# Performance work log

Measured on AMD Instinct MI355X. Metric: run time of the kernel, lower is better.

The kernel has to match this reference:

```python
import jax, jax.numpy as jnp
import numpy as np

# Reconstructed laminar V1-V2 dynamics (submodule sources were not provided;
# dynamics follow the documented dependency order L4 -> PV -> V2 -> template -> SOM -> L2/3).
N = 36            # n_orientations
H = 128           # v2_hidden_dim
DT_TAU = 0.1      # dt/tau for rate units
DT_TAU_A = 0.02   # dt/tau for adaptation
BETA_A = 0.5      # adaptation strength
W_PV = 1.0        # PV (divisive-ish subtractive) inhibition weight
W_SOM = 0.8       # SOM inhibition weight
FB_GAIN = 0.5     # feedback center-excitation gain
ALPHA = 1.0       # error-signal template subtraction
FB_SCALE = 1.0    # feedback_scale buffer


def _ring_kernel(key, n, scale):
    return scale * jax.random.normal(key, (n, n), dtype=jnp.float32)


def setup_inputs() -> dict:
    key = jax.random.key(0)
    ks = jax.random.split(key, 16)
    B, T = 1024, 512
    D_in = 2 * N + 2  # 74 packed width
    s = 1.0 / np.sqrt(N)
    sh = 1.0 / np.sqrt(D_in + H)
    return {
        "packed_input": jax.random.normal(ks[0], (B, T, D_in), dtype=jnp.float32),
        "W_l4": _ring_kernel(ks[1], N, s),
        "W_l23": _ring_kernel(ks[2], N, s),
        "W_som": _ring_kernel(ks[3], N, s),
        "Wz": sh * jax.random.normal(ks[4], (D_in + H, H), dtype=jnp.float32),
        "Wr": sh * jax.random.normal(ks[5], (D_in + H, H), dtype=jnp.float32),
        "Wh": sh * jax.random.normal(ks[6], (D_in + H, H), dtype=jnp.float32),
        "bz": jnp.zeros((H,), jnp.float32),
        "br": jnp.zeros((H,), jnp.float32),
        "bh": jnp.zeros((H,), jnp.float32),
        "Wq": (1.0 / np.sqrt(H)) * jax.random.normal(ks[7], (H, N), dtype=jnp.float32),
        "bq": jnp.zeros((N,), jnp.float32),
        "Wp": (1.0 / np.sqrt(H)) * jax.random.normal(ks[8], (H, 1), dtype=jnp.float32),
        "bp": jnp.zeros((1,), jnp.float32),
        "Ws": (1.0 / np.sqrt(H)) * jax.random.normal(ks[9], (H, 3), dtype=jnp.float32),
        "bs": jnp.zeros((3,), jnp.float32),
    }


def _forward(packed_input, W_l4, W_l23, W_som, Wz, Wr, Wh, bz, br, bh,
             Wq, bq, Wp, bp, Ws, bs):
    B, T, _ = packed_input.shape
    stim_seq = packed_input[..., :N]          # [B,T,N]
    cue_seq = packed_input[..., N:2 * N]      # [B,T,N]
    task_seq = packed_input[..., 2 * N:]      # [B,T,2]

    def gru(x, h):
        xh = jnp.concatenate([x, h], axis=-1)
        z = jax.nn.sigmoid(xh @ Wz + bz)
        r = jax.nn.sigmoid(xh @ Wr + br)
        xrh = jnp.concatenate([x, r * h], axis=-1)
        hh = jnp.tanh(xrh @ Wh + bh)
        return (1.0 - z) * h + z * hh

    def step(state, inp):
        r_l4, r_l23, r_pv, r_som, adapt, h_v2 = state
        stimulus, cue, task_state = inp
        # --- V1 L4 ring (with adaptation, PV inhibition) ---
        drive_l4 = stimulus + r_l4 @ W_l4.T - W_PV * r_pv - adapt
        r_l4_n = r_l4 + DT_TAU * (-r_l4 + jax.nn.relu(drive_l4))
        adapt_n = adapt + DT_TAU_A * (-adapt + BETA_A * r_l4_n)
        # --- PV pool (single unit per batch) ---
        pv_in = jnp.mean(r_l4_n, axis=-1, keepdims=True) + jnp.mean(r_l23, axis=-1, keepdims=True)
        r_pv_n = r_pv + DT_TAU * (-r_pv + jax.nn.relu(pv_in))
        # --- V2 context module (uses r_l23 at t-1) ---
        v2_in = jnp.concatenate([r_l23, cue, task_state], axis=-1)  # [B,74]
        h_v2_n = gru(v2_in, h_v2)
        q_pred = jax.nn.softmax(h_v2_n @ Wq + bq, axis=-1)          # [B,N]
        pi_raw = jax.nn.sigmoid(h_v2_n @ Wp + bp)                   # [B,1]
        state_logits = h_v2_n @ Ws + bs                              # [B,3]
        pi_eff = pi_raw * FB_SCALE
        # --- deep template + feedback signals ---
        deep_tmpl = q_pred * pi_eff
        som_drive = q_pred * pi_eff
        r_som_n = r_som + DT_TAU * (-r_som + jax.nn.relu(som_drive + r_som @ W_som.T))
        tmpl_mod = 1.0 + FB_GAIN * q_pred * pi_eff
        l4_to_l23 = r_l4_n - ALPHA * deep_tmpl
        # --- V1 L2/3 ring ---
        drive_l23 = l4_to_l23 * tmpl_mod + r_l23 @ W_l23.T - W_SOM * r_som_n - W_PV * r_pv_n
        r_l23_n = r_l23 + DT_TAU * (-r_l23 + jax.nn.relu(drive_l23))
        new_state = (r_l4_n, r_l23_n, r_pv_n, r_som_n, adapt_n, h_v2_n)
        return new_state, r_l23_n

    z = jnp.zeros((B, N), jnp.float32)
    init = (z, z, jnp.zeros((B, 1), jnp.float32), z, z, jnp.zeros((B, H), jnp.float32))
    inputs = (jnp.swapaxes(stim_seq, 0, 1), jnp.swapaxes(cue_seq, 0, 1), jnp.swapaxes(task_seq, 0, 1))
    _, r_l23_all = jax.lax.scan(step, init, inputs)  # [T,B,N]
    return jnp.swapaxes(r_l23_all, 0, 1)             # [B,T,N]


def reference(packed_input, W_l4, W_l23, W_som, Wz, Wr, Wh, bz, br, bh,
              Wq, bq, Wp, bp, Ws, bs):
    return _forward(packed_input, W_l4, W_l23, W_som, Wz, Wr, Wh, bz, br, bh,
                    Wq, bq, Wp, bp, Ws, bs)
```

## Files before the change

### kernel.cpp

```cpp
#include <hip/hip_runtime.h>
#include <cstdint>
#include <cstddef>


#define NN   36
#define HH   128
#define DIN  74
#define KT   202
#define KP   232
#define TT   512
#define RPB  4
#define NPAD 40
#define WSTR 44
#define HSTR 136
#define S2   6

typedef short bf16x8 __attribute__((ext_vector_type(8)));
typedef float f32x4  __attribute__((ext_vector_type(4)));

#define MFMA(a,b,c) __builtin_amdgcn_mfma_f32_16x16x32_bf16((a),(b),(c),0,0,0)
#define BAR() asm volatile("s_waitcnt lgkmcnt(0)\n\ts_barrier" ::: "memory")

__device__ __forceinline__ float fastrcp(float x) { return __builtin_amdgcn_rcpf(x); }
__device__ __forceinline__ float sigmf(float x) { return fastrcp(1.0f + __expf(-x)); }
__device__ __forceinline__ float tanhf_fast(float x) {
    return 1.0f - 2.0f * fastrcp(1.0f + __expf(2.0f * x));
}

__device__ __forceinline__ short f2bf(float v) {
    union { float f; unsigned u; } x; x.f = v;
    unsigned r = (x.u + 0x7fffu + ((x.u >> 16) & 1u)) >> 16;
    return (short)r;
}
__device__ __forceinline__ float bf2f(short s) {
    union { unsigned u; float f; } y; y.u = ((unsigned)(unsigned short)s) << 16;
    return y.f;
}

__device__ __forceinline__ unsigned cvtpk(float a, float b) {
    unsigned r;
    asm("v_cvt_pk_bf16_f32 %0, %1, %2" : "=v"(r) : "v"(a), "v"(b));
    return r;
}
__device__ __forceinline__ float lo16f(unsigned p) { return __uint_as_float(p << 16); }
__device__ __forceinline__ float hi16f(unsigned p) { return __uint_as_float(p & 0xffff0000u); }

#define DPP_STEP_MAX(x, ctrl) \
    x = fmaxf(x, __int_as_float(__builtin_amdgcn_update_dpp(0, __float_as_int(x), (ctrl), 0xF, 0xF, true)))
#define DPP_STEP_SUM(x, ctrl) \
    x = x + __int_as_float(__builtin_amdgcn_update_dpp(0, __float_as_int(x), (ctrl), 0xF, 0xF, true))

__device__ __forceinline__ float red16_max(float x) {
    DPP_STEP_MAX(x, 0xB1);
    DPP_STEP_MAX(x, 0x4E);
    DPP_STEP_MAX(x, 0x141);
    DPP_STEP_MAX(x, 0x140);
    return x;
}
__device__ __forceinline__ float red16_sum(float x) {
    DPP_STEP_SUM(x, 0xB1);
    DPP_STEP_SUM(x, 0x4E);
    DPP_STEP_SUM(x, 0x141);
    DPP_STEP_SUM(x, 0x140);
    return x;
}

#define HEADBASE 86016
#define FRAG_TOTAL 92160

extern "C" __global__ void __launch_bounds__(256)
init_frags(const float* __restrict__ Wz, const float* __restrict__ Wr,
           const float* __restrict__ Wh, const float* __restrict__ Wq,
           const float* __restrict__ Wp, short* __restrict__ frag)
{
    int idx = blockIdx.x * 256 + threadIdx.x;
    if (idx >= FRAG_TOTAL) return;
    float v;
    if (idx < HEADBASE) {
        int T = idx / 3584; int rem = idx - T * 3584;
        int s = rem >> 9;   int e = rem & 511;
        int l = e >> 3, j = e & 7;
        int k = s * 32 + ((l >> 4) << 3) + j;
        int n = ((T & 7) << 4) + (l & 15);
        const float* W = (T < 8) ? Wz : (T < 16) ? Wr : Wh;
        v = (k < KT) ? W[k * HH + n] : 0.f;
    } else {
        int r2 = idx - HEADBASE;
        int ts = r2 >> 9; int e = r2 & 511;
        int t = ts >> 2, s = ts & 3;
        int l = e >> 3, j = e & 7;
        int k = s * 32 + ((l >> 4) << 3) + j;
        int c = (t << 4) + (l & 15);
        v = (c < NN) ? Wq[k * NN + c] : (c == NN ? Wp[k] : 0.f);
    }
    frag[idx] = f2bf(v);
}

extern "C" __global__ void __launch_bounds__(1024, 4)
laminar_kernel(const float* __restrict__ packed,
               const float* __restrict__ Wl4,
               const float* __restrict__ Wl23,
               const float* __restrict__ Wsom,
               const float* __restrict__ bz,
               const float* __restrict__ br,
               const float* __restrict__ bh,
               const float* __restrict__ bq,
               const float* __restrict__ bp,
               const short* __restrict__ frag,
               float* __restrict__ out)
{
    const int tid  = threadIdx.x;
    const int r0   = blockIdx.x * RPB;
    const int lane = tid & 63;
    const int w    = tid >> 6;
    const int m    = lane & 15;
    const int q    = lane >> 4;
    const int arow = m & 7;
    const int ab   = arow >> 1;
    const int ap   = arow & 1;
    const int b0i  = (q & 1) << 1;
    const int b1i  = b0i + 1;

    __shared__ __align__(16) short xa[2][RPB][KP];
    __shared__ __align__(16) short xb[2][RPB][KP];
    __shared__ __align__(16) short hb[2][RPB][HSTR];
    __shared__ float hS[HH][S2];
    __shared__ float zgS[HH][S2];
    __shared__ float preq[48][S2];
    __shared__ __align__(16) float Wl4S[NN * WSTR], Wl23S[NN * WSTR], WsomS[NN * WSTR];
    __shared__ __align__(16) float l4s[RPB][NPAD], l23s[RPB][NPAD];
    __shared__ __align__(16) float soms[RPB][NPAD], adL[RPB][NPAD];
    __shared__ __align__(16) float l4part[RPB][NPAD];
    __shared__ __align__(16) float l23dotS[RPB][NPAD];
    __shared__ __align__(16) float somdotS[RPB][NPAD];
    __shared__ float bzL[HH], brL[HH], bhL[HH], bqL[48];
    __shared__ float pvL[RPB];
    __shared__ float bpS;

    for (int i = tid; i < HH; i += 1024) { bzL[i] = bz[i]; brL[i] = br[i]; bhL[i] = bh[i]; }
    for (int i = tid; i < 48; i += 1024) bqL[i] = (i < NN) ? bq[i] : 0.f;
    if (tid == 0) bpS = bp[0];
    for (int idx = tid; idx < NN * NN; idx += 1024) {
        const int i = idx / NN, j = idx - i * NN;
        Wl4S[i * WSTR + j]  = Wl4[idx];
        Wl23S[i * WSTR + j] = Wl23[idx];
        WsomS[i * WSTR + j] = Wsom[idx];
    }
    { short* p = (short*)xa; for (int i = tid; i < 2*RPB*KP; i += 1024) p[i] = 0; }
    { short* p = (short*)xb; for (int i = tid; i < 2*RPB*KP; i += 1024) p[i] = 0; }
    { short* p = (short*)hb; for (int i = tid; i < 2*RPB*HSTR; i += 1024) p[i] = 0; }
    { float* p = (float*)hS; for (int i = tid; i < HH*S2; i += 1024) p[i] = 0.f; }
    { float* p = (float*)l4s; for (int i = tid; i < RPB*NPAD; i += 1024) {
        p[i] = 0.f; ((float*)l23s)[i] = 0.f; ((float*)soms)[i] = 0.f;
        ((float*)adL)[i] = 0.f; ((float*)l23dotS)[i] = 0.f; ((float*)somdotS)[i] = 0.f; } }
    if (tid < RPB) pvL[tid] = 0.f;
    if (tid < RPB * NN) {
        const int r = tid / NN, i = tid - (tid / NN) * NN;
        l4part[r][i] = packed[((size_t)(r0 + r) * TT + 0) * DIN + i];
    }

    bf16x8 FA[7], FB[7];
    if (w < 8) {
        const short* a0 = frag + (w * 7) * 512 + lane * 8;
        const short* b0 = frag + ((8 + w) * 7) * 512 + lane * 8;
        #pragma unroll
        for (int s = 0; s < 7; ++s) {
            FA[s] = *(const bf16x8*)(a0 + s * 512);
            FB[s] = *(const bf16x8*)(b0 + s * 512);
        }
    } else {
        const int hw8 = w - 8;
        const short* a0 = frag + ((16 + hw8) * 7) * 512 + lane * 8;
        #pragma unroll
        for (int s = 0; s < 7; ++s) FA[s] = *(const bf16x8*)(a0 + s * 512);
        const int hw = (hw8 < 3) ? hw8 : 0;
        const short* b0 = frag + HEADBASE + (hw * 4) * 512 + lane * 8;
        #pragma unroll
        for (int s = 0; s < 4; ++s) FB[s] = *(const bf16x8*)(b0 + s * 512);
        FB[4] = FA[4]; FB[5] = FA[5]; FB[6] = FA[6];
    }

    const int  idA   = (w - 8) * 64 + lane;
    const bool isDotA = (w >= 8 && w < 11) && (idA < 144);
    const int  dvA = isDotA ? idA : 0;
    const int  drA = dvA / 36, diA = dvA - drA * 36;
    const float* dAW = Wl23S + diA * WSTR;
    const float* dAS = &l23s[drA][0];
    float*       dAD = &l23dotS[drA][diA];
    const int  idB   = (w - 13) * 64 + lane;
    const bool isL4f = (w >= 13) && (idB < 144);
    const int  lvB = isL4f ? idB : 0;
    const int  lr = lvB / 36, li = lvB - (lvB / 36) * 36;
    const int  idC   = w * 64 + lane;
    const bool isDotC = (w < 3) && (idC < 144);
    const int  cvC = isDotC ? idC : 0;
    const int  crC = cvC / 36, ciC = cvC - crC * 36;
    const float* dCW = WsomS + ciC * WSTR;
    const float* dCS = &soms[crC][0];
    float*       dCD = &somdotS[crC][ciC];
    const int  idD   = (w - 3) * 64 + lane;
    const bool isL4p = (w >= 3 && w < 6) && (idD < 144);
    const int  pvD = isL4p ? idD : 0;
    const int  prD = pvD / 36, piD = pvD - prD * 36;
    const float* pW = Wl4S + piD * WSTR;
    const float* pS = &l4s[prD][0];
    float*       pD = &l4part[prD][piD];
    const int  idE   = (w - 6) * 64 + lane;
    const bool isCue = (w >= 6 && w < 8) && (idE < 76);
    const int  evE = isCue ? idE : 0;
    const int  ctr = evE / 19;
    const int  ctc = 36 + 2 * (evE - ctr * 19);

    float ctv0 = 0.f, ctv1 = 0.f, stimreg = 0.f;
    if (isCue) {
        const size_t base0 = ((size_t)(r0 + ctr) * TT + 0) * DIN;
        #pragma unroll
        for (int d = 0; d < 2; ++d) {
            const float v = packed[base0 + ctc + d];
            const short hi = f2bf(v), lo = f2bf(v - bf2f(hi));
            xa[0][ctr][ctc + d] = hi; xa[1][ctr][ctc + d] = lo;
            if (ctc + d >= 64) { xb[0][ctr][ctc + d] = hi; xb[1][ctr][ctc + d] = lo; }
        }
        const size_t base1 = ((size_t)(r0 + ctr) * TT + 1) * DIN;
        ctv0 = packed[base1 + ctc]; ctv1 = packed[base1 + ctc + 1];
    }
    if (isL4f) stimreg = packed[((size_t)(r0 + lr) * TT + 1) * DIN + li];
    __syncthreads();

    for (int t = 0; t < TT; ++t) {
        if (w < 8) {
            const short* xaRow = &xa[ap][ab][0];
            bf16x8 Ax[7];
            #pragma unroll
            for (int s = 0; s < 7; ++s)
                Ax[s] = *(const bf16x8*)&xaRow[s * 32 + q * 8];
            f32x4 az = {0.f,0.f,0.f,0.f}, ar = {0.f,0.f,0.f,0.f};
            #pragma unroll
            for (int s = 0; s < 7; ++s) {
                az = MFMA(Ax[s], FA[s], az);
                ar = MFMA(Ax[s], FB[s], ar);
            }
            if (lane < 32) {
                const int f = w * 16 + m;
                const float z0 = az[0] + az[1], z1 = az[2] + az[3];
                const float r0v = ar[0] + ar[1], r1v = ar[2] + ar[3];
                zgS[f][b0i] = sigmf(z0 + bzL[f]);
                zgS[f][b1i] = sigmf(z1 + bzL[f]);
                const float ra = sigmf(r0v + brL[f]) * hS[f][b0i];
                const float rb = sigmf(r1v + brL[f]) * hS[f][b1i];
                const unsigned ph = cvtpk(ra, rb);
                const unsigned pl = cvtpk(ra - lo16f(ph), rb - hi16f(ph));
                xb[0][b0i][DIN + f] = (short)ph;         xb[1][b0i][DIN + f] = (short)pl;
                xb[0][b1i][DIN + f] = (short)(ph >> 16); xb[1][b1i][DIN + f] = (short)(pl >> 16);
            }
        } else if (isDotA) {
            float acc = 0.f;
            #pragma unroll
            for (int j = 0; j < NN; j += 4) {
                const float4 sv = *(const float4*)&dAS[j];
                const float4 wv = *(const float4*)&dAW[j];
                acc += sv.x*wv.x + sv.y*wv.y + sv.z*wv.z + sv.w*wv.w;
            }
            *dAD = acc;
        } else if (isL4f) {
            const float nl4 = 0.9f * l4s[lr][li]
                            + 0.1f * fmaxf(l4part[lr][li] - pvL[lr], 0.f);
            l4s[lr][li] = nl4;
            const float ad = 0.98f * adL[lr][li] + 0.01f * nl4;
            adL[lr][li] = ad;
            l4part[lr][li] = stimreg - ad;
            const int tn = (t + 2 < TT) ? t + 2 : TT - 1;
            stimreg = packed[((size_t)(r0 + lr) * TT + tn) * DIN + li];
        }
        BAR();

        if (w >= 8) {
            const short* xaRow = &xa[ap][ab][0];
            const short* xbRow = &xb[ap][ab][0];
            bf16x8 Op[7];
            Op[0] = *(const bf16x8*)&xaRow[q * 8];
            Op[1] = *(const bf16x8*)&xaRow[32 + q * 8];
            #pragma unroll
            for (int s = 2; s < 7; ++s)
                Op[s] = *(const bf16x8*)&xbRow[s * 32 + q * 8];
            f32x4 a = {0.f,0.f,0.f,0.f}, b = {0.f,0.f,0.f,0.f};
            a = MFMA(Op[0], FA[0], a);
            b = MFMA(Op[1], FA[1], b);
            a = MFMA(Op[2], FA[2], a);
            b = MFMA(Op[3], FA[3], b);
            a = MFMA(Op[4], FA[4], a);
            b = MFMA(Op[5], FA[5], b);
            a = MFMA(Op[6], FA[6], a);
            a = a + b;
            if (lane < 32) {
                const int f = (w - 8) * 16 + m;
                const float s0 = a[0] + a[1], s1 = a[2] + a[3];
                const float hh0 = tanhf_fast(s0 + bhL[f]);
                const float hh1 = tanhf_fast(s1 + bhL[f]);
                const float zg0 = zgS[f][b0i], zg1 = zgS[f][b1i];
                const float hn0 = (1.0f - zg0) * hS[f][b0i] + zg0 * hh0;
                const float hn1 = (1.0f - zg1) * hS[f][b1i] + zg1 * hh1;
                hS[f][b0i] = hn0; hS[f][b1i] = hn1;
                const unsigned ph = cvtpk(hn0, hn1);
                const unsigned pl = cvtpk(hn0 - lo16f(ph), hn1 - hi16f(ph));
                hb[0][b0i][f] = (short)ph;         hb[1][b0i][f] = (short)pl;
                hb[0][b1i][f] = (short)(ph >> 16); hb[1][b1i][f] = (short)(pl >> 16);
                xa[0][b0i][DIN + f] = (short)ph;         xa[1][b0i][DIN + f] = (short)pl;
                xa[0][b1i][DIN + f] = (short)(ph >> 16); xa[1][b1i][DIN + f] = (short)(pl >> 16);
            }
        } else if (isDotC) {
            float acc = 0.f;
            #pragma unroll
            for (int j = 0; j < NN; j += 4) {
                const float4 sv = *(const float4*)&dCS[j];
                const float4 wv = *(const float4*)&dCW[j];
                acc += sv.x*wv.x + sv.y*wv.y + sv.z*wv.z + sv.w*wv.w;
            }
            *dCD = acc;
        } else if (w == 6) {
            const int row = q;
            float s = l4s[row][m] + l23s[row][m] + l4s[row][m + 16] + l23s[row][m + 16];
            if (m < 4) s += l4s[row][m + 32] + l23s[row][m + 32];
            s = red16_sum(s);
            if (m == 0) pvL[row] = 0.9f * pvL[row] + 0.1f * fmaxf(s * (1.0f / 36.0f), 0.f);
        }
        BAR();

        if (w >= 8 && w < 11) {
            const short* hbRow = &hb[ap][ab][0];
            bf16x8 Hk[4];
            #pragma unroll
            for (int s = 0; s < 4; ++s)
                Hk[s] = *(const bf16x8*)&hbRow[s * 32 + q * 8];
            f32x4 a = {0.f,0.f,0.f,0.f};
            #pragma unroll
            for (int s = 0; s < 4; ++s) a = MFMA(Hk[s], FB[s], a);
            if (lane < 32) {
                const int c = (w - 8) * 16 + m;
                preq[c][b0i] = a[0] + a[1];
                preq[c][b1i] = a[2] + a[3];
            }
        } else if (isL4p) {
            float acc = *pD;
            #pragma unroll
            for (int j = 0; j < NN; j += 4) {
                const float4 sv = *(const float4*)&pS[j];
                const float4 wv = *(const float4*)&pW[j];
                acc += sv.x*wv.x + sv.y*wv.y + sv.z*wv.z + sv.w*wv.w;
            }
            *pD = acc;
        } else if (isCue) {
            const unsigned ph = cvtpk(ctv0, ctv1);
            const unsigned pl = cvtpk(ctv0 - lo16f(ph), ctv1 - hi16f(ph));
            xa[0][ctr][ctc]     = (short)ph;         xa[1][ctr][ctc]     = (short)pl;
            xa[0][ctr][ctc + 1] = (short)(ph >> 16); xa[1][ctr][ctc + 1] = (short)(pl >> 16);
            if (ctc >= 64) {
                xb[0][ctr][ctc]     = (short)ph;         xb[1][ctr][ctc]     = (short)pl;
                xb[0][ctr][ctc + 1] = (short)(ph >> 16); xb[1][ctr][ctc + 1] = (short)(pl >> 16);
            }
            const int tn = (t + 2 < TT) ? t + 2 : TT - 1;
            const size_t base = ((size_t)(r0 + ctr) * TT + tn) * DIN;
            ctv0 = packed[base + ctc]; ctv1 = packed[base + ctc + 1];
        }
        BAR();

        if (w < 4) {
            const int rr = w;
            const float v0 = preq[m][rr] + bqL[m];
            const float v1 = preq[m + 16][rr] + bqL[m + 16];
            const float v2 = (m < 4) ? (preq[m + 32][rr] + bqL[m + 32]) : -1e30f;
            const float pi = sigmf(preq[36][rr] + bpS);
            const float mx = red16_max(fmaxf(fmaxf(v0, v1), v2));
            const float e0 = __expf(v0 - mx);
            const float e1 = __expf(v1 - mx);
            const float e2 = (m < 4) ? __expf(v2 - mx) : 0.f;
            const float ss = red16_sum(e0 + e1 + e2);
            const float sc = fastrcp(ss) * pi;
            if (lane < 16) {
                const float pv = pvL[rr];
                const size_t outb = ((size_t)(r0 + rr) * TT + t) * NN;
                float ln01[2];
                #pragma unroll
                for (int t2 = 0; t2 < 2; ++t2) {
                    const int i = m + 16 * t2;
                    const float dt = (t2 ? e1 : e0) * sc;
                    const float sn = 0.9f * soms[rr][i]
                                   + 0.1f * fmaxf(dt + somdotS[rr][i], 0.f);
                    soms[rr][i] = sn;
                    const float acc2 = (l4s[rr][i] - dt) * (1.0f + 0.5f * dt)
                                     + l23dotS[rr][i] - 0.8f * sn - pv;
                    const float ln = 0.9f * l23s[rr][i] + 0.1f * fmaxf(acc2, 0.f);
                    l23s[rr][i] = ln;
                    out[outb + i] = ln;
                    ln01[t2] = ln;
                }
                const unsigned ph = cvtpk(ln01[0], ln01[1]);
                const unsigned pl = cvtpk(ln01[0] - lo16f(ph), ln01[1] - hi16f(ph));
                xa[0][rr][m]      = (short)ph;         xa[1][rr][m]      = (short)pl;
                xa[0][rr][m + 16] = (short)(ph >> 16); xa[1][rr][m + 16] = (short)(pl >> 16);
                if (m < 4) {
                    const int i = m + 32;
                    const float dt = e2 * sc;
                    const float sn = 0.9f * soms[rr][i]
                                   + 0.1f * fmaxf(dt + somdotS[rr][i], 0.f);
                    soms[rr][i] = sn;
                    const float acc2 = (l4s[rr][i] - dt) * (1.0f + 0.5f * dt)
                                     + l23dotS[rr][i] - 0.8f * sn - pv;
                    const float ln = 0.9f * l23s[rr][i] + 0.1f * fmaxf(acc2, 0.f);
                    l23s[rr][i] = ln;
                    out[outb + i] = ln;
                    const short hi2 = f2bf(ln);
                    xa[0][rr][i] = hi2; xa[1][rr][i] = f2bf(ln - bf2f(hi2));
                }
            }
        }
        BAR();
    }
}

extern "C" void kernel_launch(void* const* d_in, const int* in_sizes, int n_in,
                              void* d_out, int out_size, void* d_ws, size_t ws_size,
                              hipStream_t stream) {
    (void)in_sizes; (void)n_in; (void)out_size; (void)ws_size;
    const float* packed = (const float*)d_in[0];
    const float* Wl4    = (const float*)d_in[1];
    const float* Wl23   = (const float*)d_in[2];
    const float* Wsom   = (const float*)d_in[3];
    const float* Wz     = (const float*)d_in[4];
    const float* Wr     = (const float*)d_in[5];
    const float* Wh     = (const float*)d_in[6];
    const float* bz     = (const float*)d_in[7];
    const float* br     = (const float*)d_in[8];
    const float* bh     = (const float*)d_in[9];
    const float* Wq     = (const float*)d_in[10];
    const float* bq     = (const float*)d_in[11];
    const float* Wp     = (const float*)d_in[12];
    const float* bp     = (const float*)d_in[13];
    float* out  = (float*)d_out;
    short* frag = (short*)d_ws;

    init_frags<<<(FRAG_TOTAL + 255) / 256, 256, 0, stream>>>(Wz, Wr, Wh, Wq, Wp, frag);
    laminar_kernel<<<256, 1024, 0, stream>>>(packed, Wl4, Wl23, Wsom,
                                             bz, br, bh, bq, bp, frag, out);
}
```

Baseline: 1.520 ms.

## Precompute non-recurrent GRU gate partials ahead of the step and rebalance wave roles

The z/r and candidate gate GEMMs are split so the K-chunks that do not depend on the hidden state from this step (cue/task and previous h) are accumulated in the previous phase. Only the two stimulus chunks are multiplied on the critical path. The ring matrices are stored in a 4-wide transposed layout for float4 dot products. Dot-product, L4 and cue-packing duties are reassigned across waves to balance the phases. This shortens the serial chain per timestep, at the cost of more complex role bookkeeping and some redundant MFMAs on the upper waves.

```diff
diff --git a/kernel.cpp b/kernel.cpp
--- a/kernel.cpp
+++ b/kernel.cpp
@@ -11,8 +11,7 @@
 #define TT   512
 #define RPB  4
 #define NPAD 40
-#define WSTR 44
-#define HSTR 136
+#define HSTR 144
 #define S2   6
 
 typedef short bf16x8 __attribute__((ext_vector_type(8)));
@@ -123,11 +122,11 @@
 
     __shared__ __align__(16) short xa[2][RPB][KP];
     __shared__ __align__(16) short xb[2][RPB][KP];
-    __shared__ __align__(16) short hb[2][RPB][HSTR];
+    __shared__ __align__(16) short hbS[2][RPB][HSTR];
     __shared__ float hS[HH][S2];
     __shared__ float zgS[HH][S2];
     __shared__ float preq[48][S2];
-    __shared__ __align__(16) float Wl4S[NN * WSTR], Wl23S[NN * WSTR], WsomS[NN * WSTR];
+    __shared__ __align__(16) float W4l4[1296], W4l23[1296], W4som[1296];
     __shared__ __align__(16) float l4s[RPB][NPAD], l23s[RPB][NPAD];
     __shared__ __align__(16) float soms[RPB][NPAD], adL[RPB][NPAD];
     __shared__ __align__(16) float l4part[RPB][NPAD];
@@ -140,24 +139,24 @@
     for (int i = tid; i < HH; i += 1024) { bzL[i] = bz[i]; brL[i] = br[i]; bhL[i] = bh[i]; }
     for (int i = tid; i < 48; i += 1024) bqL[i] = (i < NN) ? bq[i] : 0.f;
     if (tid == 0) bpS = bp[0];
-    for (int idx = tid; idx < NN * NN; idx += 1024) {
-        const int i = idx / NN, j = idx - i * NN;
-        Wl4S[i * WSTR + j]  = Wl4[idx];
-        Wl23S[i * WSTR + j] = Wl23[idx];
-        WsomS[i * WSTR + j] = Wsom[idx];
-    }
-    { short* p = (short*)xa; for (int i = tid; i < 2*RPB*KP; i += 1024) p[i] = 0; }
-    { short* p = (short*)xb; for (int i = tid; i < 2*RPB*KP; i += 1024) p[i] = 0; }
-    { short* p = (short*)hb; for (int i = tid; i < 2*RPB*HSTR; i += 1024) p[i] = 0; }
-    { float* p = (float*)hS; for (int i = tid; i < HH*S2; i += 1024) p[i] = 0.f; }
-    { float* p = (float*)l4s; for (int i = tid; i < RPB*NPAD; i += 1024) {
+    for (int idx = tid; idx < 324; idx += 1024) {
+        const int c = idx / NN, i = idx - c * NN;
+        const int o = idx * 4;
+        #pragma unroll
+        for (int d = 0; d < 4; ++d) {
+            W4l4[o + d]  = Wl4[i * NN + 4 * c + d];
+            W4l23[o + d] = Wl23[i * NN + 4 * c + d];
+            W4som[o + d] = Wsom[i * NN + 4 * c + d];
+        }
+    }
+    { short* p = (short*)xa;  for (int i = tid; i < 2*RPB*KP;   i += 1024) p[i] = 0; }
+    { short* p = (short*)xb;  for (int i = tid; i < 2*RPB*KP;   i += 1024) p[i] = 0; }
+    { short* p = (short*)hbS; for (int i = tid; i < 2*RPB*HSTR; i += 1024) p[i] = 0; }
+    { float* p = (float*)hS;  for (int i = tid; i < HH*S2;      i += 1024) p[i] = 0.f; }
+    { float* p = (float*)l4s; for (int i = tid; i < RPB*NPAD;   i += 1024) {
         p[i] = 0.f; ((float*)l23s)[i] = 0.f; ((float*)soms)[i] = 0.f;
         ((float*)adL)[i] = 0.f; ((float*)l23dotS)[i] = 0.f; ((float*)somdotS)[i] = 0.f; } }
     if (tid < RPB) pvL[tid] = 0.f;
-    if (tid < RPB * NN) {
-        const int r = tid / NN, i = tid - (tid / NN) * NN;
-        l4part[r][i] = packed[((size_t)(r0 + r) * TT + 0) * DIN + i];
-    }
 
     bf16x8 FA[7], FB[7];
     if (w < 8) {
@@ -180,89 +179,111 @@
         FB[4] = FA[4]; FB[5] = FA[5]; FB[6] = FA[6];
     }
 
-    const int  idA   = (w - 8) * 64 + lane;
-    const bool isDotA = (w >= 8 && w < 11) && (idA < 144);
-    const int  dvA = isDotA ? idA : 0;
-    const int  drA = dvA / 36, diA = dvA - drA * 36;
-    const float* dAW = Wl23S + diA * WSTR;
-    const float* dAS = &l23s[drA][0];
-    float*       dAD = &l23dotS[drA][diA];
-    const int  idB   = (w - 13) * 64 + lane;
-    const bool isL4f = (w >= 13) && (idB < 144);
-    const int  lvB = isL4f ? idB : 0;
-    const int  lr = lvB / 36, li = lvB - (lvB / 36) * 36;
-    const int  idC   = w * 64 + lane;
-    const bool isDotC = (w < 3) && (idC < 144);
-    const int  cvC = isDotC ? idC : 0;
-    const int  crC = cvC / 36, ciC = cvC - crC * 36;
-    const float* dCW = WsomS + ciC * WSTR;
-    const float* dCS = &soms[crC][0];
-    float*       dCD = &somdotS[crC][ciC];
-    const int  idD   = (w - 3) * 64 + lane;
-    const bool isL4p = (w >= 3 && w < 6) && (idD < 144);
-    const int  pvD = isL4p ? idD : 0;
-    const int  prD = pvD / 36, piD = pvD - prD * 36;
-    const float* pW = Wl4S + piD * WSTR;
-    const float* pS = &l4s[prD][0];
-    float*       pD = &l4part[prD][piD];
-    const int  idE   = (w - 6) * 64 + lane;
-    const bool isCue = (w >= 6 && w < 8) && (idE < 76);
-    const int  evE = isCue ? idE : 0;
-    const int  ctr = evE / 19;
-    const int  ctc = 36 + 2 * (evE - ctr * 19);
-
-    float ctv0 = 0.f, ctv1 = 0.f, stimreg = 0.f;
-    if (isCue) {
-        const size_t base0 = ((size_t)(r0 + ctr) * TT + 0) * DIN;
-        #pragma unroll
-        for (int d = 0; d < 2; ++d) {
-            const float v = packed[base0 + ctc + d];
-            const short hi = f2bf(v), lo = f2bf(v - bf2f(hi));
-            xa[0][ctr][ctc + d] = hi; xa[1][ctr][ctc + d] = lo;
-            if (ctc + d >= 64) { xb[0][ctr][ctc + d] = hi; xb[1][ctr][ctc + d] = lo; }
-        }
-        const size_t base1 = ((size_t)(r0 + ctr) * TT + 1) * DIN;
-        ctv0 = packed[base1 + ctc]; ctv1 = packed[base1 + ctc + 1];
+    const int  idA = (w - 13) * 64 + lane;
+    const bool isDotA = (w >= 13) && (idA < 144);
+    const int  vA = isDotA ? idA : 0;
+    const int  drA = vA / 36, diA = vA - drA * 36;
+    const int  idB = (w - 8) * 32 + (lane - 32);
+    const bool isL4f = (w >= 8 && w < 13) && (lane >= 32) && (idB < 144);
+    const int  vB = isL4f ? idB : 0;
+    const int  lr = vB / 36, li = vB - lr * 36;
+    const int  idC = w * 64 + lane;
+    const bool isL4p = (w < 3) && (idC < 144);
+    const int  vC = isL4p ? idC : 0;
+    const int  prD = vC / 36, piD = vC - prD * 36;
+    const int  idD = (w - 3) * 64 + lane;
+    const bool isDotC = (w >= 3 && w < 6) && (idD < 144);
+    const int  vD = isDotC ? idD : 0;
+    const int  crC = vD / 36, ciC = vD - crC * 36;
+    const bool isCueA = (w == 7) && (lane < 52);
+    const int  caR = lane / 13, caC0 = 36 + 3 * (lane - caR * 13);
+    const bool isCueB = (w == 11) && (lane < 40);
+    const int  cbR = lane / 10, cbC = 64 + (lane - cbR * 10);
+
+    __syncthreads();
+
+    float cav0 = 0.f, cav1 = 0.f, cav2 = 0.f, cbv = 0.f, stimreg = 0.f;
+    if (isCueA) {
+        const size_t base0 = ((size_t)(r0 + caR) * TT + 0) * DIN;
+        #pragma unroll
+        for (int d = 0; d < 3; ++d) {
+            const int c = caC0 + d;
+            if (c < DIN) {
+                const float v = packed[base0 + c];
+                const short hi = f2bf(v);
+                xa[0][caR][c] = hi; xa[1][caR][c] = f2bf(v - bf2f(hi));
+            }
+        }
+        const size_t base1 = ((size_t)(r0 + caR) * TT + 1) * DIN;
+        cav0 = packed[base1 + caC0];
+        cav1 = (caC0 + 1 < DIN) ? packed[base1 + caC0 + 1] : 0.f;
+        cav2 = (caC0 + 2 < DIN) ? packed[base1 + caC0 + 2] : 0.f;
+    }
+    if (isCueB) {
+        const float v = packed[((size_t)(r0 + cbR) * TT + 0) * DIN + cbC];
+        const short hi = f2bf(v);
+        xb[0][cbR][cbC] = hi; xb[1][cbR][cbC] = f2bf(v - bf2f(hi));
+        cbv = packed[((size_t)(r0 + cbR) * TT + 1) * DIN + cbC];
     }
     if (isL4f) stimreg = packed[((size_t)(r0 + lr) * TT + 1) * DIN + li];
+    if (tid < RPB * NN) {
+        const int r = tid / NN, i = tid - (tid / NN) * NN;
+        l4part[r][i] = packed[((size_t)(r0 + r) * TT + 0) * DIN + i];
+    }
     __syncthreads();
 
+    f32x4 accA = {0.f,0.f,0.f,0.f}, accB = {0.f,0.f,0.f,0.f};
+    if (w < 8) {
+        const short* xaRow = &xa[ap][ab][0];
+        #pragma unroll
+        for (int s = 2; s < 7; ++s) {
+            const bf16x8 Ax = *(const bf16x8*)&xaRow[s * 32 + q * 8];
+            accA = MFMA(Ax, FA[s], accA);
+            accB = MFMA(Ax, FB[s], accB);
+        }
+    }
+    __syncthreads();
+
     for (int t = 0; t < TT; ++t) {
-        if (w < 8) {
+        {
             const short* xaRow = &xa[ap][ab][0];
-            bf16x8 Ax[7];
-            #pragma unroll
-            for (int s = 0; s < 7; ++s)
-                Ax[s] = *(const bf16x8*)&xaRow[s * 32 + q * 8];
-            f32x4 az = {0.f,0.f,0.f,0.f}, ar = {0.f,0.f,0.f,0.f};
-            #pragma unroll
-            for (int s = 0; s < 7; ++s) {
-                az = MFMA(Ax[s], FA[s], az);
-                ar = MFMA(Ax[s], FB[s], ar);
-            }
-            if (lane < 32) {
-                const int f = w * 16 + m;
-                const float z0 = az[0] + az[1], z1 = az[2] + az[3];
-                const float r0v = ar[0] + ar[1], r1v = ar[2] + ar[3];
-                zgS[f][b0i] = sigmf(z0 + bzL[f]);
-                zgS[f][b1i] = sigmf(z1 + bzL[f]);
-                const float ra = sigmf(r0v + brL[f]) * hS[f][b0i];
-                const float rb = sigmf(r1v + brL[f]) * hS[f][b1i];
-                const unsigned ph = cvtpk(ra, rb);
-                const unsigned pl = cvtpk(ra - lo16f(ph), rb - hi16f(ph));
-                xb[0][b0i][DIN + f] = (short)ph;         xb[1][b0i][DIN + f] = (short)pl;
-                xb[0][b1i][DIN + f] = (short)(ph >> 16); xb[1][b1i][DIN + f] = (short)(pl >> 16);
-            }
-        } else if (isDotA) {
+            const bf16x8 A0 = *(const bf16x8*)&xaRow[q * 8];
+            const bf16x8 A1 = *(const bf16x8*)&xaRow[32 + q * 8];
+            if (w < 8) {
+                accA = MFMA(A0, FA[0], accA);
+                accB = MFMA(A0, FB[0], accB);
+                accA = MFMA(A1, FA[1], accA);
+                accB = MFMA(A1, FB[1], accB);
+                if (lane < 32) {
+                    const int f = w * 16 + m;
+                    const float z0 = accA[0] + accA[1], z1 = accA[2] + accA[3];
+                    const float r0v = accB[0] + accB[1], r1v = accB[2] + accB[3];
+                    zgS[f][b0i] = sigmf(z0 + bzL[f]);
+                    zgS[f][b1i] = sigmf(z1 + bzL[f]);
+                    const float ra = sigmf(r0v + brL[f]) * hS[f][b0i];
+                    const float rb = sigmf(r1v + brL[f]) * hS[f][b1i];
+                    const unsigned ph = cvtpk(ra, rb);
+                    const unsigned pl = cvtpk(ra - lo16f(ph), rb - hi16f(ph));
+                    xb[0][b0i][DIN + f] = (short)ph;         xb[1][b0i][DIN + f] = (short)pl;
+                    xb[0][b1i][DIN + f] = (short)(ph >> 16); xb[1][b1i][DIN + f] = (short)(pl >> 16);
+                }
+            } else {
+                const f32x4 z4 = {0.f,0.f,0.f,0.f};
+                accA = MFMA(A0, FA[0], z4);
+                accB = MFMA(A1, FA[1], z4);
+            }
+        }
+        if (isDotA) {
             float acc = 0.f;
             #pragma unroll
-            for (int j = 0; j < NN; j += 4) {
-                const float4 sv = *(const float4*)&dAS[j];
-                const float4 wv = *(const float4*)&dAW[j];
+            for (int c = 0; c < 9; ++c) {
+                const float4 wv = *(const float4*)&W4l23[(c * NN + diA) * 4];
+                const float4 sv = *(const float4*)&l23s[drA][4 * c];
                 acc += sv.x*wv.x + sv.y*wv.y + sv.z*wv.z + sv.w*wv.w;
             }
-            *dAD = acc;
-        } else if (isL4f) {
+            l23dotS[drA][diA] = acc;
+        }
+        if (isL4f) {
             const float nl4 = 0.9f * l4s[lr][li]
                             + 0.1f * fmaxf(l4part[lr][li] - pvL[lr], 0.f);
             l4s[lr][li] = nl4;
@@ -275,23 +296,17 @@
         BAR();
 
         if (w >= 8) {
-            const short* xaRow = &xa[ap][ab][0];
             const short* xbRow = &xb[ap][ab][0];
-            bf16x8 Op[7];
-            Op[0] = *(const bf16x8*)&xaRow[q * 8];
-            Op[1] = *(const bf16x8*)&xaRow[32 + q * 8];
-            #pragma unroll
-            for (int s = 2; s < 7; ++s)
-                Op[s] = *(const bf16x8*)&xbRow[s * 32 + q * 8];
-            f32x4 a = {0.f,0.f,0.f,0.f}, b = {0.f,0.f,0.f,0.f};
-            a = MFMA(Op[0], FA[0], a);
-            b = MFMA(Op[1], FA[1], b);
-            a = MFMA(Op[2], FA[2], a);
-            b = MFMA(Op[3], FA[3], b);
-            a = MFMA(Op[4], FA[4], a);
-            b = MFMA(Op[5], FA[5], b);
-            a = MFMA(Op[6], FA[6], a);
-            a = a + b;
+            bf16x8 Op[5];
+            #pragma unroll
+            for (int s = 0; s < 5; ++s)
+                Op[s] = *(const bf16x8*)&xbRow[(s + 2) * 32 + q * 8];
+            accA = MFMA(Op[0], FA[2], accA);
+            accB = MFMA(Op[1], FA[3], accB);
+            accA = MFMA(Op[2], FA[4], accA);
+            accB = MFMA(Op[3], FA[5], accB);
+            accA = MFMA(Op[4], FA[6], accA);
+            const f32x4 a = accA + accB;
             if (lane < 32) {
                 const int f = (w - 8) * 16 + m;
                 const float s0 = a[0] + a[1], s1 = a[2] + a[3];
@@ -303,64 +318,81 @@
                 hS[f][b0i] = hn0; hS[f][b1i] = hn1;
                 const unsigned ph = cvtpk(hn0, hn1);
                 const unsigned pl = cvtpk(hn0 - lo16f(ph), hn1 - hi16f(ph));
-                hb[0][b0i][f] = (short)ph;         hb[1][b0i][f] = (short)pl;
-                hb[0][b1i][f] = (short)(ph >> 16); hb[1][b1i][f] = (short)(pl >> 16);
+                hbS[0][b0i][f] = (short)ph;         hbS[1][b0i][f] = (short)pl;
+                hbS[0][b1i][f] = (short)(ph >> 16); hbS[1][b1i][f] = (short)(pl >> 16);
                 xa[0][b0i][DIN + f] = (short)ph;         xa[1][b0i][DIN + f] = (short)pl;
                 xa[0][b1i][DIN + f] = (short)(ph >> 16); xa[1][b1i][DIN + f] = (short)(pl >> 16);
             }
+        } else if (isL4p) {
+            float acc = l4part[prD][piD];
+            #pragma unroll
+            for (int c = 0; c < 9; ++c) {
+                const float4 wv = *(const float4*)&W4l4[(c * NN + piD) * 4];
+                const float4 sv = *(const float4*)&l4s[prD][4 * c];
+                acc += sv.x*wv.x + sv.y*wv.y + sv.z*wv.z + sv.w*wv.w;
+            }
+            l4part[prD][piD] = acc;
         } else if (isDotC) {
             float acc = 0.f;
             #pragma unroll
-            for (int j = 0; j < NN; j += 4) {
-                const float4 sv = *(const float4*)&dCS[j];
-                const float4 wv = *(const float4*)&dCW[j];
+            for (int c = 0; c < 9; ++c) {
+                const float4 wv = *(const float4*)&W4som[(c * NN + ciC) * 4];
+                const float4 sv = *(const float4*)&soms[crC][4 * c];
                 acc += sv.x*wv.x + sv.y*wv.y + sv.z*wv.z + sv.w*wv.w;
             }
-            *dCD = acc;
+            somdotS[crC][ciC] = acc;
         } else if (w == 6) {
             const int row = q;
             float s = l4s[row][m] + l23s[row][m] + l4s[row][m + 16] + l23s[row][m + 16];
             if (m < 4) s += l4s[row][m + 32] + l23s[row][m + 32];
             s = red16_sum(s);
             if (m == 0) pvL[row] = 0.9f * pvL[row] + 0.1f * fmaxf(s * (1.0f / 36.0f), 0.f);
+        } else if (isCueA) {
+            #pragma unroll
+            for (int d = 0; d < 3; ++d) {
+                const int c = caC0 + d;
+                if (c < DIN) {
+                    const float v = (d == 0) ? cav0 : (d == 1) ? cav1 : cav2;
+                    const short hi = f2bf(v);
+                    xa[0][caR][c] = hi; xa[1][caR][c] = f2bf(v - bf2f(hi));
+                }
+            }
+            const int tn = (t + 2 < TT) ? t + 2 : TT - 1;
+            const size_t base = ((size_t)(r0 + caR) * TT + tn) * DIN;
+            cav0 = packed[base + caC0];
+            cav1 = (caC0 + 1 < DIN) ? packed[base + caC0 + 1] : 0.f;
+            cav2 = (caC0 + 2 < DIN) ? packed[base + caC0 + 2] : 0.f;
         }
         BAR();
 
-        if (w >= 8 && w < 11) {
-            const short* hbRow = &hb[ap][ab][0];
-            bf16x8 Hk[4];
-            #pragma unroll
-            for (int s = 0; s < 4; ++s)
-                Hk[s] = *(const bf16x8*)&hbRow[s * 32 + q * 8];
-            f32x4 a = {0.f,0.f,0.f,0.f};
-            #pragma unroll
-            for (int s = 0; s < 4; ++s) a = MFMA(Hk[s], FB[s], a);
+        if (w < 8) {
+            const short* xaRow = &xa[ap][ab][0];
+            const f32x4 z4 = {0.f,0.f,0.f,0.f};
+            accA = z4; accB = z4;
+            #pragma unroll
+            for (int s = 2; s < 7; ++s) {
+                const bf16x8 Ax = *(const bf16x8*)&xaRow[s * 32 + q * 8];
+                accA = MFMA(Ax, FA[s], accA);
+                accB = MFMA(Ax, FB[s], accB);
+            }
+        } else if (w < 11) {
+            const short* hbRow = &hbS[ap][ab][0];
+            f32x4 hd = {0.f,0.f,0.f,0.f};
+            #pragma unroll
+            for (int s = 0; s < 4; ++s) {
+                const bf16x8 Hk = *(const bf16x8*)&hbRow[s * 32 + q * 8];
+                hd = MFMA(Hk, FB[s], hd);
+            }
             if (lane < 32) {
                 const int c = (w - 8) * 16 + m;
-                preq[c][b0i] = a[0] + a[1];
-                preq[c][b1i] = a[2] + a[3];
-            }
-        } else if (isL4p) {
-            float acc = *pD;
-            #pragma unroll
-            for (int j = 0; j < NN; j += 4) {
-                const float4 sv = *(const float4*)&pS[j];
-                const float4 wv = *(const float4*)&pW[j];
-                acc += sv.x*wv.x + sv.y*wv.y + sv.z*wv.z + sv.w*wv.w;
-            }
-            *pD = acc;
-        } else if (isCue) {
-            const unsigned ph = cvtpk(ctv0, ctv1);
-            const unsigned pl = cvtpk(ctv0 - lo16f(ph), ctv1 - hi16f(ph));
-            xa[0][ctr][ctc]     = (short)ph;         xa[1][ctr][ctc]     = (short)pl;
-            xa[0][ctr][ctc + 1] = (short)(ph >> 16); xa[1][ctr][ctc + 1] = (short)(pl >> 16);
-            if (ctc >= 64) {
-                xb[0][ctr][ctc]     = (short)ph;         xb[1][ctr][ctc]     = (short)pl;
-                xb[0][ctr][ctc + 1] = (short)(ph >> 16); xb[1][ctr][ctc + 1] = (short)(pl >> 16);
-            }
+                preq[c][b0i] = hd[0] + hd[1];
+                preq[c][b1i] = hd[2] + hd[3];
+            }
+        } else if (isCueB) {
+            const short hi = f2bf(cbv);
+            xb[0][cbR][cbC] = hi; xb[1][cbR][cbC] = f2bf(cbv - bf2f(hi));
             const int tn = (t + 2 < TT) ? t + 2 : TT - 1;
-            const size_t base = ((size_t)(r0 + ctr) * TT + tn) * DIN;
-            ctv0 = packed[base + ctc]; ctv1 = packed[base + ctc + 1];
+            cbv = packed[((size_t)(r0 + cbR) * TT + tn) * DIN + cbC];
         }
         BAR();
 
```

Measured after the change: 1.785 ms. 1.17x slower.

## Skew L4 update one step ahead with double-buffered state and interleaved ring weights

Applied to the files above, without the earlier changes.

Moves the L4 rate and adaptation update from the first phase into the last phase of the timestep, computing the next step's L4 into a double-buffered array. The prologue now seeds step 0 directly, so the L4 chain runs one step ahead and its serial dependency leaves the first phase. The ring weight matrices are re-laid out in 4-column interleaved chunks so lanes read contiguous float4s. The z-gate sigmoid is also deferred to the phase where it is consumed. This rebalances per-phase work across waves and shortens the first phase, at the cost of more complex state bookkeeping and an added prologue barrier.

```diff
diff --git a/kernel.cpp b/kernel.cpp
--- a/kernel.cpp
+++ b/kernel.cpp
@@ -11,7 +11,6 @@
 #define TT   512
 #define RPB  4
 #define NPAD 40
-#define WSTR 44
 #define HSTR 136
 #define S2   6
 
@@ -123,12 +122,13 @@
 
     __shared__ __align__(16) short xa[2][RPB][KP];
     __shared__ __align__(16) short xb[2][RPB][KP];
-    __shared__ __align__(16) short hb[2][RPB][HSTR];
+    __shared__ __align__(16) short hbS[2][RPB][HSTR];
     __shared__ float hS[HH][S2];
     __shared__ float zgS[HH][S2];
     __shared__ float preq[48][S2];
-    __shared__ __align__(16) float Wl4S[NN * WSTR], Wl23S[NN * WSTR], WsomS[NN * WSTR];
-    __shared__ __align__(16) float l4s[RPB][NPAD], l23s[RPB][NPAD];
+    __shared__ __align__(16) float W4l4[1296], W4l23[1296], W4som[1296];
+    __shared__ __align__(16) float l4s[2][RPB][NPAD];
+    __shared__ __align__(16) float l23s[RPB][NPAD];
     __shared__ __align__(16) float soms[RPB][NPAD], adL[RPB][NPAD];
     __shared__ __align__(16) float l4part[RPB][NPAD];
     __shared__ __align__(16) float l23dotS[RPB][NPAD];
@@ -140,24 +140,25 @@
     for (int i = tid; i < HH; i += 1024) { bzL[i] = bz[i]; brL[i] = br[i]; bhL[i] = bh[i]; }
     for (int i = tid; i < 48; i += 1024) bqL[i] = (i < NN) ? bq[i] : 0.f;
     if (tid == 0) bpS = bp[0];
-    for (int idx = tid; idx < NN * NN; idx += 1024) {
-        const int i = idx / NN, j = idx - i * NN;
-        Wl4S[i * WSTR + j]  = Wl4[idx];
-        Wl23S[i * WSTR + j] = Wl23[idx];
-        WsomS[i * WSTR + j] = Wsom[idx];
-    }
-    { short* p = (short*)xa; for (int i = tid; i < 2*RPB*KP; i += 1024) p[i] = 0; }
-    { short* p = (short*)xb; for (int i = tid; i < 2*RPB*KP; i += 1024) p[i] = 0; }
-    { short* p = (short*)hb; for (int i = tid; i < 2*RPB*HSTR; i += 1024) p[i] = 0; }
-    { float* p = (float*)hS; for (int i = tid; i < HH*S2; i += 1024) p[i] = 0.f; }
-    { float* p = (float*)l4s; for (int i = tid; i < RPB*NPAD; i += 1024) {
-        p[i] = 0.f; ((float*)l23s)[i] = 0.f; ((float*)soms)[i] = 0.f;
-        ((float*)adL)[i] = 0.f; ((float*)l23dotS)[i] = 0.f; ((float*)somdotS)[i] = 0.f; } }
+    for (int idx = tid; idx < 324; idx += 1024) {
+        const int c = idx / NN, i = idx - c * NN;
+        const int o = idx * 4;
+        #pragma unroll
+        for (int d = 0; d < 4; ++d) {
+            W4l4[o + d]  = Wl4[i * NN + 4 * c + d];
+            W4l23[o + d] = Wl23[i * NN + 4 * c + d];
+            W4som[o + d] = Wsom[i * NN + 4 * c + d];
+        }
+    }
+    { short* p = (short*)xa;  for (int i = tid; i < 2*RPB*KP;   i += 1024) p[i] = 0; }
+    { short* p = (short*)xb;  for (int i = tid; i < 2*RPB*KP;   i += 1024) p[i] = 0; }
+    { short* p = (short*)hbS; for (int i = tid; i < 2*RPB*HSTR; i += 1024) p[i] = 0; }
+    { float* p = (float*)hS;  for (int i = tid; i < HH*S2;      i += 1024) p[i] = 0.f; }
+    { float* p = (float*)l4s; for (int i = tid; i < 2*RPB*NPAD; i += 1024) p[i] = 0.f; }
+    { float* p = (float*)l23s; for (int i = tid; i < RPB*NPAD;  i += 1024) {
+        p[i] = 0.f; ((float*)soms)[i] = 0.f; ((float*)adL)[i] = 0.f;
+        ((float*)l23dotS)[i] = 0.f; ((float*)somdotS)[i] = 0.f; } }
     if (tid < RPB) pvL[tid] = 0.f;
-    if (tid < RPB * NN) {
-        const int r = tid / NN, i = tid - (tid / NN) * NN;
-        l4part[r][i] = packed[((size_t)(r0 + r) * TT + 0) * DIN + i];
-    }
 
     bf16x8 FA[7], FB[7];
     if (w < 8) {
@@ -180,38 +181,49 @@
         FB[4] = FA[4]; FB[5] = FA[5]; FB[6] = FA[6];
     }
 
-    const int  idA   = (w - 8) * 64 + lane;
-    const bool isDotA = (w >= 8 && w < 11) && (idA < 144);
-    const int  dvA = isDotA ? idA : 0;
-    const int  drA = dvA / 36, diA = dvA - drA * 36;
-    const float* dAW = Wl23S + diA * WSTR;
+    const int  idA = (w - 13) * 64 + lane;
+    const bool isDotA = (w >= 13) && (idA < 144);
+    const int  vA = idA < 144 ? (idA < 0 ? 0 : idA) : 0;
+    const int  drA = (isDotA ? vA : 0) / 36, diA = (isDotA ? vA : 0) - drA * 36;
+    const float* dAW = W4l23 + diA * 4;
     const float* dAS = &l23s[drA][0];
     float*       dAD = &l23dotS[drA][diA];
-    const int  idB   = (w - 13) * 64 + lane;
-    const bool isL4f = (w >= 13) && (idB < 144);
-    const int  lvB = isL4f ? idB : 0;
-    const int  lr = lvB / 36, li = lvB - (lvB / 36) * 36;
-    const int  idC   = w * 64 + lane;
+    const int  idB = (w - 8) * 64 + lane;
+    const bool isL4f = (w >= 8 && w < 11) && (idB < 144);
+    const int  vB = isL4f ? idB : 0;
+    const int  lr = vB / 36, li = vB - lr * 36;
+    const int  idC = w * 64 + lane;
     const bool isDotC = (w < 3) && (idC < 144);
-    const int  cvC = isDotC ? idC : 0;
-    const int  crC = cvC / 36, ciC = cvC - crC * 36;
-    const float* dCW = WsomS + ciC * WSTR;
+    const int  vC = isDotC ? idC : 0;
+    const int  crC = vC / 36, ciC = vC - crC * 36;
+    const float* dCW = W4som + ciC * 4;
     const float* dCS = &soms[crC][0];
     float*       dCD = &somdotS[crC][ciC];
-    const int  idD   = (w - 3) * 64 + lane;
+    const int  idD = (w - 3) * 64 + lane;
     const bool isL4p = (w >= 3 && w < 6) && (idD < 144);
-    const int  pvD = isL4p ? idD : 0;
-    const int  prD = pvD / 36, piD = pvD - prD * 36;
-    const float* pW = Wl4S + piD * WSTR;
-    const float* pS = &l4s[prD][0];
-    float*       pD = &l4part[prD][piD];
-    const int  idE   = (w - 6) * 64 + lane;
+    const int  vD = isL4p ? idD : 0;
+    const int  prD = vD / 36, piD = vD - prD * 36;
+    const float* pW = W4l4 + piD * 4;
+    const int  idE = (w - 6) * 64 + lane;
     const bool isCue = (w >= 6 && w < 8) && (idE < 76);
     const int  evE = isCue ? idE : 0;
     const int  ctr = evE / 19;
     const int  ctc = 36 + 2 * (evE - ctr * 19);
 
+    __syncthreads();
+
     float ctv0 = 0.f, ctv1 = 0.f, stimreg = 0.f;
+    if (tid < RPB * NN) {
+        const int r = tid / NN, i = tid - (tid / NN) * NN;
+        const size_t b = ((size_t)(r0 + r) * TT) * DIN + i;
+        const float s0 = packed[b];
+        const float nl4 = 0.1f * fmaxf(s0, 0.f);
+        l4s[0][r][i] = nl4;
+        const float ad = 0.01f * nl4;
+        adL[r][i] = ad;
+        l4part[r][i] = packed[b + DIN] - ad;
+    }
+    if (isL4f) stimreg = packed[((size_t)(r0 + lr) * TT + 2) * DIN + li];
     if (isCue) {
         const size_t base0 = ((size_t)(r0 + ctr) * TT + 0) * DIN;
         #pragma unroll
@@ -224,10 +236,12 @@
         const size_t base1 = ((size_t)(r0 + ctr) * TT + 1) * DIN;
         ctv0 = packed[base1 + ctc]; ctv1 = packed[base1 + ctc + 1];
     }
-    if (isL4f) stimreg = packed[((size_t)(r0 + lr) * TT + 1) * DIN + li];
     __syncthreads();
 
     for (int t = 0; t < TT; ++t) {
+        float (*l4cur)[NPAD] = l4s[t & 1];
+        float (*l4nxt)[NPAD] = l4s[(t + 1) & 1];
+
         if (w < 8) {
             const short* xaRow = &xa[ap][ab][0];
             bf16x8 Ax[7];
@@ -244,8 +258,8 @@
                 const int f = w * 16 + m;
                 const float z0 = az[0] + az[1], z1 = az[2] + az[3];
                 const float r0v = ar[0] + ar[1], r1v = ar[2] + ar[3];
-                zgS[f][b0i] = sigmf(z0 + bzL[f]);
-                zgS[f][b1i] = sigmf(z1 + bzL[f]);
+                zgS[f][b0i] = z0 + bzL[f];
+                zgS[f][b1i] = z1 + bzL[f];
                 const float ra = sigmf(r0v + brL[f]) * hS[f][b0i];
                 const float rb = sigmf(r1v + brL[f]) * hS[f][b1i];
                 const unsigned ph = cvtpk(ra, rb);
@@ -256,21 +270,12 @@
         } else if (isDotA) {
             float acc = 0.f;
             #pragma unroll
-            for (int j = 0; j < NN; j += 4) {
-                const float4 sv = *(const float4*)&dAS[j];
-                const float4 wv = *(const float4*)&dAW[j];
+            for (int c = 0; c < 9; ++c) {
+                const float4 wv = *(const float4*)&dAW[c * 144];
+                const float4 sv = *(const float4*)&dAS[4 * c];
                 acc += sv.x*wv.x + sv.y*wv.y + sv.z*wv.z + sv.w*wv.w;
             }
             *dAD = acc;
-        } else if (isL4f) {
-            const float nl4 = 0.9f * l4s[lr][li]
-                            + 0.1f * fmaxf(l4part[lr][li] - pvL[lr], 0.f);
-            l4s[lr][li] = nl4;
-            const float ad = 0.98f * adL[lr][li] + 0.01f * nl4;
-            adL[lr][li] = ad;
-            l4part[lr][li] = stimreg - ad;
-            const int tn = (t + 2 < TT) ? t + 2 : TT - 1;
-            stimreg = packed[((size_t)(r0 + lr) * TT + tn) * DIN + li];
         }
         BAR();
 
@@ -297,37 +302,38 @@
                 const float s0 = a[0] + a[1], s1 = a[2] + a[3];
                 const float hh0 = tanhf_fast(s0 + bhL[f]);
                 const float hh1 = tanhf_fast(s1 + bhL[f]);
-                const float zg0 = zgS[f][b0i], zg1 = zgS[f][b1i];
+                const float zg0 = sigmf(zgS[f][b0i]);
+                const float zg1 = sigmf(zgS[f][b1i]);
                 const float hn0 = (1.0f - zg0) * hS[f][b0i] + zg0 * hh0;
                 const float hn1 = (1.0f - zg1) * hS[f][b1i] + zg1 * hh1;
                 hS[f][b0i] = hn0; hS[f][b1i] = hn1;
                 const unsigned ph = cvtpk(hn0, hn1);
                 const unsigned pl = cvtpk(hn0 - lo16f(ph), hn1 - hi16f(ph));
-                hb[0][b0i][f] = (short)ph;         hb[1][b0i][f] = (short)pl;
-                hb[0][b1i][f] = (short)(ph >> 16); hb[1][b1i][f] = (short)(pl >> 16);
+                hbS[0][b0i][f] = (short)ph;         hbS[1][b0i][f] = (short)pl;
+                hbS[0][b1i][f] = (short)(ph >> 16); hbS[1][b1i][f] = (short)(pl >> 16);
                 xa[0][b0i][DIN + f] = (short)ph;         xa[1][b0i][DIN + f] = (short)pl;
                 xa[0][b1i][DIN + f] = (short)(ph >> 16); xa[1][b1i][DIN + f] = (short)(pl >> 16);
             }
         } else if (isDotC) {
             float acc = 0.f;
             #pragma unroll
-            for (int j = 0; j < NN; j += 4) {
-                const float4 sv = *(const float4*)&dCS[j];
-                const float4 wv = *(const float4*)&dCW[j];
+            for (int c = 0; c < 9; ++c) {
+                const float4 wv = *(const float4*)&dCW[c * 144];
+                const float4 sv = *(const float4*)&dCS[4 * c];
                 acc += sv.x*wv.x + sv.y*wv.y + sv.z*wv.z + sv.w*wv.w;
             }
             *dCD = acc;
         } else if (w == 6) {
             const int row = q;
-            float s = l4s[row][m] + l23s[row][m] + l4s[row][m + 16] + l23s[row][m + 16];
-            if (m < 4) s += l4s[row][m + 32] + l23s[row][m + 32];
+            float s = l4cur[row][m] + l23s[row][m] + l4cur[row][m + 16] + l23s[row][m + 16];
+            if (m < 4) s += l4cur[row][m + 32] + l23s[row][m + 32];
             s = red16_sum(s);
             if (m == 0) pvL[row] = 0.9f * pvL[row] + 0.1f * fmaxf(s * (1.0f / 36.0f), 0.f);
         }
         BAR();
 
         if (w >= 8 && w < 11) {
-            const short* hbRow = &hb[ap][ab][0];
+            const short* hbRow = &hbS[ap][ab][0];
             bf16x8 Hk[4];
             #pragma unroll
             for (int s = 0; s < 4; ++s)
@@ -341,14 +347,15 @@
                 preq[c][b1i] = a[2] + a[3];
             }
         } else if (isL4p) {
-            float acc = *pD;
-            #pragma unroll
-            for (int j = 0; j < NN; j += 4) {
-                const float4 sv = *(const float4*)&pS[j];
-                const float4 wv = *(const float4*)&pW[j];
+            const float* pS = &l4cur[prD][0];
+            float acc = l4part[prD][piD];
+            #pragma unroll
+            for (int c = 0; c < 9; ++c) {
+                const float4 wv = *(const float4*)&pW[c * 144];
+                const float4 sv = *(const float4*)&pS[4 * c];
                 acc += sv.x*wv.x + sv.y*wv.y + sv.z*wv.z + sv.w*wv.w;
             }
-            *pD = acc;
+            l4part[prD][piD] = acc;
         } else if (isCue) {
             const unsigned ph = cvtpk(ctv0, ctv1);
             const unsigned pl = cvtpk(ctv0 - lo16f(ph), ctv1 - hi16f(ph));
@@ -387,7 +394,7 @@
                     const float sn = 0.9f * soms[rr][i]
                                    + 0.1f * fmaxf(dt + somdotS[rr][i], 0.f);
                     soms[rr][i] = sn;
-                    const float acc2 = (l4s[rr][i] - dt) * (1.0f + 0.5f * dt)
+                    const float acc2 = (l4cur[rr][i] - dt) * (1.0f + 0.5f * dt)
                                      + l23dotS[rr][i] - 0.8f * sn - pv;
                     const float ln = 0.9f * l23s[rr][i] + 0.1f * fmaxf(acc2, 0.f);
                     l23s[rr][i] = ln;
@@ -404,7 +411,7 @@
                     const float sn = 0.9f * soms[rr][i]
                                    + 0.1f * fmaxf(dt + somdotS[rr][i], 0.f);
                     soms[rr][i] = sn;
-                    const float acc2 = (l4s[rr][i] - dt) * (1.0f + 0.5f * dt)
+                    const float acc2 = (l4cur[rr][i] - dt) * (1.0f + 0.5f * dt)
                                      + l23dotS[rr][i] - 0.8f * sn - pv;
                     const float ln = 0.9f * l23s[rr][i] + 0.1f * fmaxf(acc2, 0.f);
                     l23s[rr][i] = ln;
@@ -413,6 +420,15 @@
                     xa[0][rr][i] = hi2; xa[1][rr][i] = f2bf(ln - bf2f(hi2));
                 }
             }
+        } else if (isL4f) {
+            const float nl4 = 0.9f * l4cur[lr][li]
+                            + 0.1f * fmaxf(l4part[lr][li] - pvL[lr], 0.f);
+            l4nxt[lr][li] = nl4;
+            const float ad = 0.98f * adL[lr][li] + 0.01f * nl4;
+            adL[lr][li] = ad;
+            l4part[lr][li] = stimreg - ad;
+            const int tn = (t + 3 < TT) ? t + 3 : TT - 1;
+            stimreg = packed[((size_t)(r0 + lr) * TT + tn) * DIN + li];
         }
         BAR();
     }
```

After: 1.416 ms. 6.8% less time.
